# Optimization experiments

Hardware: AMD Instinct MI355X
Metric: run time of the kernel (lower is better)

Reference implementation:

```python
import jax, jax.numpy as jnp
import numpy as np

# static config (matches init_kwargs)
H = 64; W = 64; WS = 8; SHIFT = 4; HEADS = 16; DIM = 512; TED = 512; B = 16
NW = (H // WS) * (W // WS)          # 64 windows
WS2 = WS * WS                        # 64 tokens per window
N = WS2 + 1                          # +1 time-embedding token appended per window
HIDDEN = int(DIM * 4.0)


def _rel_pos_index():
    # standard Swin relative-position index over the WS*WS window tokens
    coords = np.stack(np.meshgrid(np.arange(WS), np.arange(WS), indexing='ij'))  # (2, WS, WS)
    cf = coords.reshape(2, -1)
    rel = (cf[:, :, None] - cf[:, None, :]).transpose(1, 2, 0)  # (WS2, WS2, 2)
    rel[..., 0] += WS - 1
    rel[..., 1] += WS - 1
    rel[..., 0] *= 2 * WS - 1
    return rel.sum(-1)  # (WS2, WS2) int


def _attn_mask():
    # shifted-window attention mask, exactly as built in __init__
    img_mask = np.zeros((H, W), dtype=np.float32)
    slices = (slice(0, -WS), slice(-WS, -SHIFT), slice(-SHIFT, None))
    cnt = 0
    for hs in slices:
        for ws_ in slices:
            img_mask[hs, ws_] = cnt
            cnt += 1
    mw = img_mask.reshape(H // WS, WS, W // WS, WS).transpose(0, 2, 1, 3).reshape(-1, WS2)  # (NW, WS2)
    diff = mw[:, None, :] - mw[:, :, None]
    return np.where(diff != 0, -100.0, 0.0).astype(np.float32)  # (NW, WS2, WS2)


def _ln(x, g, b):
    m = x.mean(-1, keepdims=True)
    v = ((x - m) ** 2).mean(-1, keepdims=True)
    return (x - m) / jnp.sqrt(v + 1e-5) * g + b


def setup_inputs() -> dict:
    key = jax.random.key(0)
    ks = jax.random.split(key, 10)
    s = 0.02
    return {
        'x': jax.random.normal(ks[0], (B, H * W, DIM), dtype=jnp.float32),
        'emb': jax.random.normal(ks[1], (B, TED), dtype=jnp.float32),
        'gamma1': jnp.ones((DIM,), jnp.float32),
        'beta1': jnp.zeros((DIM,), jnp.float32),
        'W_emb': jax.random.normal(ks[2], (TED, DIM), jnp.float32) * s,
        'b_emb': jnp.zeros((DIM,), jnp.float32),
        'W_qkv': jax.random.normal(ks[3], (DIM, 3 * DIM), jnp.float32) * s,
        'b_qkv': jnp.zeros((3 * DIM,), jnp.float32),
        'rel_bias_table': jax.random.normal(ks[4], ((2 * WS - 1) ** 2, HEADS), jnp.float32) * s,
        'W_proj': jax.random.normal(ks[5], (DIM, DIM), jnp.float32) * s,
        'b_proj': jnp.zeros((DIM,), jnp.float32),
        'gamma2': jnp.ones((DIM,), jnp.float32),
        'beta2': jnp.zeros((DIM,), jnp.float32),
        'W1': jax.random.normal(ks[6], (DIM, HIDDEN), jnp.float32) * s,
        'b1': jnp.zeros((HIDDEN,), jnp.float32),
        'W2': jax.random.normal(ks[7], (HIDDEN, DIM), jnp.float32) * s,
        'b2': jnp.zeros((DIM,), jnp.float32),
    }


def reference(x, emb, gamma1, beta1, W_emb, b_emb, W_qkv, b_qkv, rel_bias_table,
              W_proj, b_proj, gamma2, beta2, W1, b1, W2, b2):
    Bb, L, C = x.shape
    hd = C // HEADS
    shortcut = x
    # norm1 -> spatial -> cyclic shift
    xn = _ln(x, gamma1, beta1).reshape(Bb, H, W, C)
    xs = jnp.roll(xn, (-SHIFT, -SHIFT), axis=(1, 2))
    # window partition: (B, NW, WS2, C)
    xw = xs.reshape(Bb, H // WS, WS, W // WS, WS, C).transpose(0, 1, 3, 2, 4, 5)
    xw = xw.reshape(Bb, NW, WS2, C)
    # append time-embedding token to each window
    t = jax.nn.silu(emb) @ W_emb + b_emb                       # (B, C)
    t = jnp.broadcast_to(t[:, None, None, :], (Bb, NW, 1, C))
    xw = jnp.concatenate([xw, t], axis=2).reshape(Bb * NW, N, C)
    # windowed multi-head attention
    qkv = (xw @ W_qkv + b_qkv).reshape(Bb * NW, N, 3, HEADS, hd).transpose(2, 0, 3, 1, 4)
    q, k, v = qkv[0] * (hd ** -0.5), qkv[1], qkv[2]            # (B*NW, HEADS, N, hd)
    attn = jnp.einsum('bhnd,bhmd->bhnm', q, k)
    bias = rel_bias_table[_rel_pos_index().reshape(-1)].reshape(WS2, WS2, HEADS).transpose(2, 0, 1)
    bias = jnp.pad(bias, ((0, 0), (0, 1), (0, 1)))             # zero bias for time token
    attn = attn + bias[None]
    mask = jnp.pad(jnp.asarray(_attn_mask()), ((0, 0), (0, 1), (0, 1)))  # (NW, N, N)
    attn = attn.reshape(Bb, NW, HEADS, N, N) + mask[None, :, None]
    attn = jax.nn.softmax(attn.reshape(Bb * NW, HEADS, N, N), axis=-1)
    out = jnp.einsum('bhnm,bhmd->bnhd', attn, v).reshape(Bb * NW, N, C)
    out = (out @ W_proj + b_proj)[:, :WS2]                     # drop time token
    # window reverse + reverse shift
    out = out.reshape(Bb, H // WS, W // WS, WS, WS, C).transpose(0, 1, 3, 2, 4, 5).reshape(Bb, H, W, C)
    out = jnp.roll(out, (SHIFT, SHIFT), axis=(1, 2)).reshape(Bb, L, C)
    x1 = shortcut + out
    # norm2 + MLP (exact GELU, as torch nn.GELU default)
    hmid = jax.nn.gelu(_ln(x1, gamma2, beta2) @ W1 + b1, approximate=False)
    return x1 + hmid @ W2 + b2
```

## Files before the change

### kernel.cpp

```cpp
#include <hip/hip_runtime.h>
#include <hip/hip_bf16.h>

typedef __hip_bfloat16 bf16;
typedef short short4_t __attribute__((ext_vector_type(4)));
typedef short short8 __attribute__((ext_vector_type(8)));
typedef float f32x4 __attribute__((ext_vector_type(4)));

#define DIMC 512
#define HEADS_ 16
#define NTOK 65
#define NWIN 64
#define NB 16
#define HID 2048
#define TOTROWS 66560
#define IMGROWS 65536
#define ATT_CHUNK_WB 128
#define ATT_CHUNK_ROWS (ATT_CHUNK_WB * NTOK)


__device__ __forceinline__ float b2f(short s) {
  unsigned int u = ((unsigned int)(unsigned short)s) << 16;
  float f; __builtin_memcpy(&f, &u, 4); return f;
}
__device__ __forceinline__ short f2s(float f) {
  bf16 b = __float2bfloat16(f);
  short s; __builtin_memcpy(&s, &b, 2); return s;
}

__device__ __forceinline__ void async_lds16(const bf16* g, bf16* l) {
  __builtin_amdgcn_global_load_lds(
      (const __attribute__((address_space(1))) unsigned int*)g,
      (__attribute__((address_space(3))) unsigned int*)l,
      16, 0, 0);
}

__device__ __forceinline__ void wave_stats512(const float* v, float& m, float& rstd)
{
  float s = 0.0f, ss = 0.0f;
  #pragma unroll
  for (int e = 0; e < 8; ++e) { s += v[e]; ss += v[e] * v[e]; }
  #pragma unroll
  for (int o = 1; o < 64; o <<= 1) { s += __shfl_xor(s, o); ss += __shfl_xor(ss, o); }
  m = s * (1.0f / 512.0f);
  rstd = rsqrtf(ss * (1.0f / 512.0f) - m * m + 1e-5f);
}

__device__ __forceinline__ float gelu_t(float v) {
  float v2 = v * v;
  float a  = fmaf(0.044715f, v2, 1.0f);
  float e  = __builtin_exp2f(-2.3022042f * (v * a));
  return v * __builtin_amdgcn_rcpf(1.0f + e);
}


__global__ __launch_bounds__(256) void time_emb_kernel(
    const float* __restrict__ emb, const float* __restrict__ W_emb,
    const float* __restrict__ b_emb, float* __restrict__ t)
{
  int b = blockIdx.x;
  int c = blockIdx.y * 256 + threadIdx.x;
  __shared__ float se[512];
  for (int k = threadIdx.x; k < 512; k += 256) {
    float e = emb[b * 512 + k];
    se[k] = e / (1.0f + expf(-e));
  }
  __syncthreads();
  float acc = b_emb[c];
  for (int k = 0; k < 512; ++k) acc += se[k] * W_emb[k * 512 + c];
  t[b * 512 + c] = acc;
}

__global__ void transpose_cast_kernel(const float* __restrict__ W, bf16* __restrict__ Wt,
                                      int Kd, int Nd)
{
  __shared__ float tile[32][33];
  int n0 = blockIdx.x * 32, k0 = blockIdx.y * 32;
  for (int r = threadIdx.y; r < 32; r += 8)
    tile[r][threadIdx.x] = W[(long)(k0 + r) * Nd + n0 + threadIdx.x];
  __syncthreads();
  for (int r = threadIdx.y; r < 32; r += 8)
    Wt[(long)(n0 + r) * Kd + k0 + threadIdx.x] = __float2bfloat16(tile[threadIdx.x][r]);
}

__global__ __launch_bounds__(256) void bias_mask_kernel(
    const float* __restrict__ btab, float* __restrict__ tbl)
{
  int h = blockIdx.x, wt = blockIdx.y;
  for (int idx = threadIdx.x; idx < 6400; idx += 256) {
    int i = idx / 80, t = idx % 80;
    float v;
    if (t >= 65) v = -1e30f;
    else if (i >= 64 || t == 64) v = 0.0f;
    else {
      int rel = (((i >> 3) - (t >> 3) + 7) * 15) + ((i & 7) - (t & 7) + 7);
      v = btab[rel * HEADS_ + h];
      int rci = (wt & 2) ? (((i >> 3) < 4) ? 1 : 2) : 0;
      int cci = (wt & 1) ? (((i & 7) < 4) ? 1 : 2) : 0;
      int rct = (wt & 2) ? (((t >> 3) < 4) ? 1 : 2) : 0;
      int cct = (wt & 1) ? (((t & 7) < 4) ? 1 : 2) : 0;
      if (rci * 3 + cci != rct * 3 + cct) v -= 100.0f;
    }
    tbl[(h * 4 + wt) * 6400 + idx] = v;
  }
}

__global__ __launch_bounds__(256) void ln1_window_kernel(
    const float* __restrict__ x, const float* __restrict__ gamma,
    const float* __restrict__ beta, const float* __restrict__ t,
    bf16* __restrict__ xw)
{
  long r = (long)blockIdx.x * 4 + (threadIdx.x >> 6);
  int lane = threadIdx.x & 63;
  int wb = (int)(r / NTOK), i = (int)(r % NTOK);
  int b = wb >> 6, w = wb & 63;
  bf16* out = xw + r * 512 + lane * 8;
  if (i == 64) {
    const float* tr = t + b * 512 + lane * 8;
    short8 o;
    #pragma unroll
    for (int e = 0; e < 8; ++e) o[e] = f2s(tr[e]);
    *(short8*)out = o;
    return;
  }
  int wh = w >> 3, ww = w & 7, ih = i >> 3, iw = i & 7;
  int hsrc = ((wh * 8 + ih) + 4) & 63;
  int wsrc = ((ww * 8 + iw) + 4) & 63;
  const float* xr = x + ((long)b * 4096 + hsrc * 64 + wsrc) * 512 + lane * 8;
  float v[8];
  *(f32x4*)&v[0] = *(const f32x4*)xr;
  *(f32x4*)&v[4] = *(const f32x4*)(xr + 4);
  float m, rstd;
  wave_stats512(v, m, rstd);
  const float* g = gamma + lane * 8;
  const float* bt = beta + lane * 8;
  short8 o;
  #pragma unroll
  for (int e = 0; e < 8; ++e) o[e] = f2s((v[e] - m) * rstd * g[e] + bt[e]);
  *(short8*)out = o;
}

__global__ __launch_bounds__(256) void ln2_kernel(
    const bf16* __restrict__ x1, const float* __restrict__ gamma,
    const float* __restrict__ beta, bf16* __restrict__ out)
{
  long r = (long)blockIdx.x * 4 + (threadIdx.x >> 6);
  int lane = threadIdx.x & 63;
  short8 xv = *(const short8*)(x1 + r * 512 + lane * 8);
  float v[8];
  #pragma unroll
  for (int e = 0; e < 8; ++e) v[e] = b2f(xv[e]);
  float m, rstd;
  wave_stats512(v, m, rstd);
  const float* g = gamma + lane * 8;
  const float* bt = beta + lane * 8;
  short8 o;
  #pragma unroll
  for (int e = 0; e < 8; ++e) o[e] = f2s((v[e] - m) * rstd * g[e] + bt[e]);
  *(short8*)(out + r * 512 + lane * 8) = o;
}

template<int EPI, int K>
__global__ __launch_bounds__(512, 1) void gemm8p_kernel(
    const bf16* __restrict__ A, const bf16* __restrict__ Bt,
    const float* __restrict__ bias, int N, int nx,
    bf16* __restrict__ outB, float* __restrict__ outF,
    const float* __restrict__ xinF, const bf16* __restrict__ xinB, int rowOffset)
{
  constexpr int NKT = K / 64;
  __shared__ bf16 lds[8][128 * 64];
  const int tid = threadIdx.x;
  const int lane = tid & 63, wv = tid >> 6;
  const int wm = wv >> 2, wn = wv & 3;
  const int fr = lane & 15, fg = lane >> 4;

  const int nwg = gridDim.x, bid = blockIdx.x;
  const int q8 = nwg >> 3, rr8 = nwg & 7;
  const int xcd = bid & 7, idx = bid >> 3;
  const int sid = (xcd < rr8 ? xcd * (q8 + 1) : rr8 * (q8 + 1) + (xcd - rr8) * q8) + idx;
  const long row0 = (long)(sid / nx) * 256;
  const long col0 = (long)(sid % nx) * 256;

  const int rl = lane >> 3, sl = lane & 7;
  const int sls = sl ^ rl;

  auto stageH = [&](int buf, int mat, int h, int kt) {
    const bf16* base = mat ? Bt : A;
    const long rb = (mat ? col0 : row0) + h * 128 + wv * 8 + rl;
    const bf16* src = base + rb * (long)K + kt + sls * 8;
    bf16* dst = &lds[buf * 4 + mat * 2 + h][(wv * 8) * 64];
    async_lds16(src, dst);
    async_lds16(src + 64 * (long)K, dst + 64 * 64);
  };
  auto fragA = [&](int buf, int h, int mi, int ks) -> short8 {
    int r = wm * 64 + mi * 16 + fr;
    return *(const short8*)((const char*)&lds[buf * 4 + h][0] + r * 128 + (((ks * 4 + fg) ^ (r & 7)) << 4));
  };
  auto fragB = [&](int buf, int h, int ni, int ks) -> short8 {
    int r = wn * 32 + ni * 16 + fr;
    return *(const short8*)((const char*)&lds[buf * 4 + 2 + h][0] + r * 128 + (((ks * 4 + fg) ^ (r & 7)) << 4));
  };

  f32x4 acc[8][4] = {};
  short8 af[4][2], bvh[2][2][2];

  stageH(0, 0, 0, 0); stageH(0, 1, 0, 0); stageH(0, 1, 1, 0); stageH(0, 0, 1, 0);

  for (int t = 0; t < NKT; ++t) {
    const int buf = t & 1, nb = buf ^ 1;
    const bool st = (t + 1 < NKT);
    const int kt2 = (t + 1) << 6;

    asm volatile("s_waitcnt vmcnt(4)" ::: "memory");
    __builtin_amdgcn_s_barrier();
    #pragma unroll
    for (int mi = 0; mi < 4; ++mi) { af[mi][0] = fragA(buf, 0, mi, 0); af[mi][1] = fragA(buf, 0, mi, 1); }
    #pragma unroll
    for (int ni = 0; ni < 2; ++ni) { bvh[0][ni][0] = fragB(buf, 0, ni, 0); bvh[0][ni][1] = fragB(buf, 0, ni, 1); }
    if (st) stageH(nb, 0, 0, kt2);
    __builtin_amdgcn_s_setprio(1);
    #pragma unroll
    for (int mi = 0; mi < 4; ++mi)
      #pragma unroll
      for (int ni = 0; ni < 2; ++ni)
        #pragma unroll
        for (int ks = 0; ks < 2; ++ks)
          acc[mi][ni] = __builtin_amdgcn_mfma_f32_16x16x32_bf16(af[mi][ks], bvh[0][ni][ks], acc[mi][ni], 0, 0, 0);
    __builtin_amdgcn_s_setprio(0);

    if (st) asm volatile("s_waitcnt vmcnt(4)" ::: "memory");
    else    asm volatile("s_waitcnt vmcnt(2)" ::: "memory");
    __builtin_amdgcn_s_barrier();
    #pragma unroll
    for (int ni = 0; ni < 2; ++ni) { bvh[1][ni][0] = fragB(buf, 1, ni, 0); bvh[1][ni][1] = fragB(buf, 1, ni, 1); }
    if (st) stageH(nb, 1, 0, kt2);
    __builtin_amdgcn_s_setprio(1);
    #pragma unroll
    for (int mi = 0; mi < 4; ++mi)
      #pragma unroll
      for (int ni = 0; ni < 2; ++ni)
        #pragma unroll
        for (int ks = 0; ks < 2; ++ks)
          acc[mi][2 + ni] = __builtin_amdgcn_mfma_f32_16x16x32_bf16(af[mi][ks], bvh[1][ni][ks], acc[mi][2 + ni], 0, 0, 0);
    __builtin_amdgcn_s_setprio(0);

    if (st) asm volatile("s_waitcnt vmcnt(4)" ::: "memory");
    else    asm volatile("s_waitcnt vmcnt(0)" ::: "memory");
    __builtin_amdgcn_s_barrier();
    #pragma unroll
    for (int mi = 0; mi < 4; ++mi) { af[mi][0] = fragA(buf, 1, mi, 0); af[mi][1] = fragA(buf, 1, mi, 1); }
    if (st) { stageH(nb, 1, 1, kt2); stageH(nb, 0, 1, kt2); }
    __builtin_amdgcn_s_setprio(1);
    #pragma unroll
    for (int mi = 0; mi < 4; ++mi)
      #pragma unroll
      for (int ni = 0; ni < 2; ++ni)
        #pragma unroll
        for (int ks = 0; ks < 2; ++ks)
          acc[4 + mi][ni] = __builtin_amdgcn_mfma_f32_16x16x32_bf16(af[mi][ks], bvh[0][ni][ks], acc[4 + mi][ni], 0, 0, 0);
    #pragma unroll
    for (int mi = 0; mi < 4; ++mi)
      #pragma unroll
      for (int ni = 0; ni < 2; ++ni)
        #pragma unroll
        for (int ks = 0; ks < 2; ++ks)
          acc[4 + mi][2 + ni] = __builtin_amdgcn_mfma_f32_16x16x32_bf16(af[mi][ks], bvh[1][ni][ks], acc[4 + mi][2 + ni], 0, 0, 0);
    __builtin_amdgcn_s_setprio(0);
  }

  if (EPI == 0 || EPI == 1) {
    float bs[2][2];
    #pragma unroll
    for (int nh = 0; nh < 2; ++nh)
      #pragma unroll
      for (int ni = 0; ni < 2; ++ni)
        bs[nh][ni] = bias[col0 + nh * 128 + wn * 32 + ni * 16 + fr];
    #pragma unroll
    for (int h = 0; h < 2; ++h)
      #pragma unroll
      for (int mi = 0; mi < 4; ++mi)
        #pragma unroll
        for (int j = 0; j < 4; ++j) {
          long rr = row0 + h * 128 + wm * 64 + mi * 16 + fg * 4 + j;
          #pragma unroll
          for (int nh = 0; nh < 2; ++nh)
            #pragma unroll
            for (int ni = 0; ni < 2; ++ni) {
              long cc = col0 + nh * 128 + wn * 32 + ni * 16 + fr;
              float v = acc[h * 4 + mi][nh * 2 + ni][j] + bs[nh][ni];
              if (EPI == 1) v = gelu_t(v);
              outB[rr * N + cc] = __float2bfloat16(v);
            }
        }
    return;
  }

  __syncthreads();
  float* ep = (float*)&lds[0][0];
  const int c64 = tid & 63, r8 = tid >> 6;
  const f32x4 b4 = *(const f32x4*)&bias[col0 + c64 * 4];
  #pragma unroll
  for (int g = 0; g < 4; ++g) {
    int h = g >> 1, wmg = g & 1;
    if (wm == wmg) {
      #pragma unroll
      for (int mi = 0; mi < 4; ++mi)
        #pragma unroll
        for (int nh = 0; nh < 2; ++nh)
          #pragma unroll
          for (int ni = 0; ni < 2; ++ni)
            #pragma unroll
            for (int j = 0; j < 4; ++j)
              ep[(mi * 16 + fg * 4 + j) * 260 + nh * 128 + wn * 32 + ni * 16 + fr] =
                  acc[h * 4 + mi][nh * 2 + ni][j];
    }
    __syncthreads();
    #pragma unroll
    for (int it = 0; it < 8; ++it) {
      int lrow = it * 8 + r8;
      long rr = row0 + h * 128 + wmg * 64 + lrow;
      f32x4 v = *(const f32x4*)&ep[lrow * 260 + c64 * 4];
      v += b4;
      if (EPI == 2) {
        int grow = rowOffset + (int)rr;
        int ii = grow % NTOK;
        if (ii != 64) {
          int wb = grow / NTOK;
          int b = wb >> 6, w = wb & 63;
          int wh = w >> 3, ww = w & 7, ih = ii >> 3, iw = ii & 7;
          int hh   = ((wh * 8 + ih) + 4) & 63;
          int wcol = ((ww * 8 + iw) + 4) & 63;
          long o = ((long)b * 4096 + hh * 64 + wcol) * 512 + col0 + c64 * 4;
          f32x4 xi = *(const f32x4*)&xinF[o];
          f32x4 x1 = xi + v;
          short4_t s4;
          #pragma unroll
          for (int e = 0; e < 4; ++e) s4[e] = f2s(x1[e]);
          *(short4_t*)&outB[o] = s4;
        }
      } else {
        long o = rr * N + col0 + c64 * 4;
        short4_t xv = *(const short4_t*)&xinB[o];
        f32x4 xf;
        #pragma unroll
        for (int e = 0; e < 4; ++e) xf[e] = b2f(xv[e]);
        *(f32x4*)&outF[o] = xf + v;
      }
    }
    __syncthreads();
  }
}

template<int EPI, int K>
__global__ __launch_bounds__(256, 3) void gemmk_kernel(
    const bf16* __restrict__ A, const bf16* __restrict__ Bt,
    const float* __restrict__ bias, int N, int nx,
    bf16* __restrict__ outB, float* __restrict__ outF,
    const float* __restrict__ xinF, const bf16* __restrict__ xinB, int rowOffset)
{
  constexpr int NKT = K / 32;
  static_assert((NKT - 1) % 3 == 0, "triplet peel needs NKT = 3m+1");
  __shared__ bf16 ldsbuf[6 * 128 * 32];
  bf16* const lAp = ldsbuf;
  bf16* const lBp = ldsbuf + 3 * 4096;
  const int tid = threadIdx.x;
  const int lane = tid & 63, wv = tid >> 6;
  const int wm = wv >> 1, wn = wv & 1;
  const int fr = lane & 15, fg = lane >> 4;

  const int nwg = gridDim.x, bid = blockIdx.x;
  const int q8 = nwg >> 3, rr8 = nwg & 7;
  const int xcd = bid & 7, idx = bid >> 3;
  const int sid = (xcd < rr8 ? xcd * (q8 + 1) : rr8 * (q8 + 1) + (xcd - rr8) * q8) + idx;
  const long row0 = (long)(sid / nx) * 128;
  const long col0 = (long)(sid % nx) * 128;

  const int rl = lane >> 2, sp = lane & 3;
  const int s = sp ^ ((rl >> 1) & 3);
  const bf16* ga0 = A  + (row0 + wv * 32 + rl) * (long)K + s * 8;
  const bf16* ga1 = ga0 + 16 * (long)K;
  const bf16* gb0 = Bt + (col0 + wv * 32 + rl) * (long)K + s * 8;
  const bf16* gb1 = gb0 + 16 * (long)K;

  f32x4 acc[4][4] = {};
  const int swr = (fg ^ ((fr >> 1) & 3)) << 4;

  auto stage = [&](int buf, int t) {
    const long o = (long)t * 32;
    async_lds16(ga0 + o, &lAp[buf * 4096 + (wv * 32) * 32]);
    async_lds16(ga1 + o, &lAp[buf * 4096 + (wv * 32 + 16) * 32]);
    async_lds16(gb0 + o, &lBp[buf * 4096 + (wv * 32) * 32]);
    async_lds16(gb1 + o, &lBp[buf * 4096 + (wv * 32 + 16) * 32]);
  };

  stage(0, 0);
  stage(1, 1);

#define GBODY(BUF)                                                              \
  do {                                                                          \
    if (t + 1 < NKT) asm volatile("s_waitcnt vmcnt(4)" ::: "memory");           \
    else             asm volatile("s_waitcnt vmcnt(0)" ::: "memory");           \
    __builtin_amdgcn_s_barrier();                                               \
    short8 bfv[4], af[4];                                                       \
    _Pragma("unroll")                                                           \
    for (int ni = 0; ni < 4; ++ni)                                              \
      bfv[ni] = *(const short8*)((const char*)&lBp[(BUF) * 4096] +              \
                                 (wn * 64 + ni * 16 + fr) * 64 + swr);          \
    _Pragma("unroll")                                                           \
    for (int mi = 0; mi < 4; ++mi)                                              \
      af[mi] = *(const short8*)((const char*)&lAp[(BUF) * 4096] +               \
                                (wm * 64 + mi * 16 + fr) * 64 + swr);           \
    if (t + 2 < NKT) stage(((BUF) + 2) % 3, t + 2);                             \
    __builtin_amdgcn_s_setprio(1);                                              \
    _Pragma("unroll")                                                           \
    for (int mi = 0; mi < 4; ++mi)                                              \
      _Pragma("unroll")                                                         \
      for (int ni = 0; ni < 4; ++ni)                                            \
        acc[mi][ni] = __builtin_amdgcn_mfma_f32_16x16x32_bf16(                  \
            af[mi], bfv[ni], acc[mi][ni], 0, 0, 0);                             \
    __builtin_amdgcn_s_setprio(0);                                              \
    ++t;                                                                        \
  } while (0)

  int t = 0;
  GBODY(0);
  for (int g = 0; g < (NKT - 1) / 3; ++g) {
    GBODY(1);
    GBODY(2);
    GBODY(0);
  }
#undef GBODY

  if (EPI == 2 || EPI == 3) {
    __syncthreads();
    float* ep = (float*)ldsbuf;
    const int l31 = lane & 31, lr2 = lane >> 5;
    const f32x4 b4 = *(const f32x4*)&bias[col0 + l31 * 4];
    #pragma unroll
    for (int h = 0; h < 2; ++h) {
      if (wm == h) {
        #pragma unroll
        for (int mi = 0; mi < 4; ++mi)
          #pragma unroll
          for (int ni = 0; ni < 4; ++ni)
            #pragma unroll
            for (int j = 0; j < 4; ++j)
              ep[(mi * 16 + fg * 4 + j) * 132 + wn * 64 + ni * 16 + fr] = acc[mi][ni][j];
      }
      __syncthreads();
      #pragma unroll
      for (int it = 0; it < 8; ++it) {
        int lrow = it * 8 + wv * 2 + lr2;
        long rr = row0 + h * 64 + lrow;
        f32x4 v = *(const f32x4*)&ep[lrow * 132 + l31 * 4];
        v += b4;
        if (EPI == 2) {
          int grow = rowOffset + (int)rr;
          int ii = grow % NTOK;
          if (ii != 64) {
            int wb = grow / NTOK;
            int b = wb >> 6, w = wb & 63;
            int wh = w >> 3, ww = w & 7, ih = ii >> 3, iw = ii & 7;
            int hh   = ((wh * 8 + ih) + 4) & 63;
            int wcol = ((ww * 8 + iw) + 4) & 63;
            long o = ((long)b * 4096 + hh * 64 + wcol) * 512 + col0 + l31 * 4;
            f32x4 xi = *(const f32x4*)&xinF[o];
            f32x4 x1 = xi + v;
            short4_t s4;
            #pragma unroll
            for (int e = 0; e < 4; ++e) s4[e] = f2s(x1[e]);
            *(short4_t*)&outB[o] = s4;
          }
        } else {
          long o = rr * N + col0 + l31 * 4;
          short4_t xv = *(const short4_t*)&xinB[o];
          f32x4 xf;
          #pragma unroll
          for (int e = 0; e < 4; ++e) xf[e] = b2f(xv[e]);
          *(f32x4*)&outF[o] = xf + v;
        }
      }
      __syncthreads();
    }
    return;
  }

  float bs[4];
  #pragma unroll
  for (int ni = 0; ni < 4; ++ni) bs[ni] = bias[col0 + wn * 64 + ni * 16 + fr];
  #pragma unroll
  for (int mi = 0; mi < 4; ++mi) {
    #pragma unroll
    for (int j = 0; j < 4; ++j) {
      long rr = row0 + wm * 64 + mi * 16 + fg * 4 + j;
      #pragma unroll
      for (int ni = 0; ni < 4; ++ni) {
        long cc = col0 + wn * 64 + ni * 16 + fr;
        float v = acc[mi][ni][j] + bs[ni];
        if (EPI == 0) {
          outB[rr * N + cc] = __float2bfloat16(v);
        } else {
          outB[rr * N + cc] = __float2bfloat16(gelu_t(v));
        }
      }
    }
  }
}

__global__ __launch_bounds__(64, 4) void attn_mfma_kernel(
    const bf16* __restrict__ qkv, bf16* __restrict__ attnO,
    const float* __restrict__ tbl, int wb0)
{
  __shared__ bf16 P[80 * 104];
  const int lwb = blockIdx.x, h = blockIdx.y;
  const int lane = threadIdx.x;
  const int fr = lane & 15, g = lane >> 4;
  const float scale = 0.17677669529663687f;
  const bf16* base = qkv + (long)lwb * 65 * 1536 + h * 32 + g * 8;

  for (int idx = lane; idx < 240; idx += 64) {
    int i = idx / 3, sl = idx % 3;
    *(short8*)&P[i * 104 + 80 + sl * 8] = (short8){0, 0, 0, 0, 0, 0, 0, 0};
  }

  short8 bq[5];
  #pragma unroll
  for (int tn = 0; tn < 5; ++tn) {
    int qr = tn * 16 + fr; qr = qr > 64 ? 64 : qr;
    bq[tn] = *(const short8*)(base + (long)qr * 1536);
  }

  f32x4 acc[5][5];
  #pragma unroll
  for (int tm = 0; tm < 5; ++tm) {
    int kr = tm * 16 + fr; kr = kr > 64 ? 64 : kr;
    short8 ak = *(const short8*)(base + 512 + (long)kr * 1536);
    #pragma unroll
    for (int tn = 0; tn < 5; ++tn)
      acc[tm][tn] = __builtin_amdgcn_mfma_f32_16x16x32_bf16(
          ak, bq[tn], (f32x4){0.0f, 0.0f, 0.0f, 0.0f}, 0, 0, 0);
  }

  const int w = (wb0 + lwb) & 63;
  const int wt = (((w >> 3) == 7) ? 2 : 0) + (((w & 7) == 7) ? 1 : 0);
  const float* tp = tbl + (h * 4 + wt) * 6400;
  #pragma unroll
  for (int tn = 0; tn < 5; ++tn) {
    const int i = tn * 16 + fr;
    const float* ti = tp + i * 80 + g * 4;
    float m = -3.0e38f;
    #pragma unroll
    for (int tm = 0; tm < 5; ++tm) {
      f32x4 bvv = *(const f32x4*)(ti + tm * 16);
      #pragma unroll
      for (int r = 0; r < 4; ++r) {
        float sv = fmaf(acc[tm][tn][r], scale, bvv[r]);
        acc[tm][tn][r] = sv;
        m = fmaxf(m, sv);
      }
    }
    m = fmaxf(m, __shfl_xor(m, 16));
    m = fmaxf(m, __shfl_xor(m, 32));
    float l = 0.0f;
    #pragma unroll
    for (int tm = 0; tm < 5; ++tm)
      #pragma unroll
      for (int r = 0; r < 4; ++r) {
        float e = __expf(acc[tm][tn][r] - m);
        acc[tm][tn][r] = e;
        l += e;
      }
    l += __shfl_xor(l, 16);
    l += __shfl_xor(l, 32);
    float inv = 1.0f / l;
    #pragma unroll
    for (int tm = 0; tm < 5; ++tm) {
      short4_t pk;
      #pragma unroll
      for (int r = 0; r < 4; ++r) pk[r] = f2s(acc[tm][tn][r] * inv);
      *(short4_t*)&P[i * 104 + tm * 16 + g * 4] = pk;
    }
  }

  const bf16* vbase = qkv + (long)lwb * 65 * 1536 + 1024 + h * 32;
  f32x4 oacc[2][5] = {};
  #pragma unroll
  for (int kt = 0; kt < 3; ++kt) {
    short8 bp[5];
    #pragma unroll
    for (int tn = 0; tn < 5; ++tn)
      bp[tn] = *(const short8*)&P[(tn * 16 + fr) * 104 + kt * 32 + g * 8];
    #pragma unroll
    for (int ma = 0; ma < 2; ++ma) {
      short8 av;
      #pragma unroll
      for (int e = 0; e < 8; ++e) {
        int vr = kt * 32 + g * 8 + e; vr = vr > 64 ? 64 : vr;
        av[e] = *(const short*)(vbase + (long)vr * 1536 + ma * 16 + fr);
      }
      #pragma unroll
      for (int tn = 0; tn < 5; ++tn)
        oacc[ma][tn] = __builtin_amdgcn_mfma_f32_16x16x32_bf16(
            av, bp[tn], oacc[ma][tn], 0, 0, 0);
    }
  }

  #pragma unroll
  for (int tn = 0; tn < 5; ++tn) {
    int i = tn * 16 + fr;
    if (i < 65) {
      bf16* op = attnO + (long)(lwb * 65 + i) * 512 + h * 32 + g * 4;
      #pragma unroll
      for (int ma = 0; ma < 2; ++ma) {
        short4_t o4;
        #pragma unroll
        for (int r = 0; r < 4; ++r) o4[r] = f2s(oacc[ma][tn][r]);
        *(short4_t*)(op + ma * 16) = o4;
      }
    }
  }
}


extern "C" void kernel_launch(void* const* d_in, const int* in_sizes, int n_in,
                              void* d_out, int out_size, void* d_ws, size_t ws_size,
                              hipStream_t stream)
{
  const float* x      = (const float*)d_in[0];
  const float* emb    = (const float*)d_in[1];
  const float* gamma1 = (const float*)d_in[2];
  const float* beta1  = (const float*)d_in[3];
  const float* W_emb  = (const float*)d_in[4];
  const float* b_emb  = (const float*)d_in[5];
  const float* W_qkv  = (const float*)d_in[6];
  const float* b_qkv  = (const float*)d_in[7];
  const float* btab   = (const float*)d_in[8];
  const float* W_proj = (const float*)d_in[9];
  const float* b_proj = (const float*)d_in[10];
  const float* gamma2 = (const float*)d_in[11];
  const float* beta2  = (const float*)d_in[12];
  const float* W1     = (const float*)d_in[13];
  const float* b1     = (const float*)d_in[14];
  const float* W2     = (const float*)d_in[15];
  const float* b2     = (const float*)d_in[16];
  float* out = (float*)d_out;
  (void)n_in; (void)in_sizes; (void)out_size;

  char* ws = (char*)d_ws;
  size_t off = 0;
  auto alloc = [&](size_t bytes) -> char* {
    char* p = ws + off;
    off += (bytes + 255) & ~(size_t)255;
    return p;
  };
  bf16* wt_qkv  = (bf16*)alloc((size_t)1536 * 512 * 2);
  bf16* wt_proj = (bf16*)alloc((size_t)512 * 512 * 2);
  bf16* wt1     = (bf16*)alloc((size_t)2048 * 512 * 2);
  bf16* wt2     = (bf16*)alloc((size_t)512 * 2048 * 2);
  float* tvec   = (float*)alloc((size_t)16 * 512 * 4);
  float* tbl    = (float*)alloc((size_t)16 * 4 * 6400 * 4);

  const size_t sz_xw    = (size_t)TOTROWS * 512 * 2;
  const size_t sz_qkv   = (size_t)TOTROWS * 1536 * 2;
  const size_t sz_attnO = (size_t)TOTROWS * 512 * 2;
  const bool big = ws_size >= off + sz_xw + sz_qkv + sz_attnO + (4u << 20);

  transpose_cast_kernel<<<dim3(1536 / 32, 512 / 32), dim3(32, 8), 0, stream>>>(W_qkv, wt_qkv, 512, 1536);
  transpose_cast_kernel<<<dim3(512 / 32, 512 / 32),  dim3(32, 8), 0, stream>>>(W_proj, wt_proj, 512, 512);
  transpose_cast_kernel<<<dim3(2048 / 32, 512 / 32), dim3(32, 8), 0, stream>>>(W1, wt1, 512, 2048);
  transpose_cast_kernel<<<dim3(512 / 32, 2048 / 32), dim3(32, 8), 0, stream>>>(W2, wt2, 2048, 512);
  time_emb_kernel<<<dim3(16, 2), 256, 0, stream>>>(emb, W_emb, b_emb, tvec);
  bias_mask_kernel<<<dim3(16, 4), 256, 0, stream>>>(btab, tbl);

  if (big) {
    char* regionA = alloc(sz_xw);
    char* regionQ = alloc(sz_qkv);
    bf16* attnO   = (bf16*)alloc(sz_attnO);
    bf16* xw   = (bf16*)regionA;
    bf16* x1b  = (bf16*)regionA;
    bf16* qkv  = (bf16*)regionQ;
    bf16* h_c  = (bf16*)regionQ;
    bf16* ln2b = (bf16*)(regionQ + (size_t)32768 * 2048 * 2);

    ln1_window_kernel<<<TOTROWS / 4, 256, 0, stream>>>(x, gamma1, beta1, tvec, xw);
    gemm8p_kernel<0, 512><<<6 * 260, 512, 0, stream>>>(
        xw, wt_qkv, b_qkv, 1536, 6, qkv, nullptr, nullptr, nullptr, 0);
    attn_mfma_kernel<<<dim3(NB * NWIN, HEADS_), 64, 0, stream>>>(qkv, attnO, tbl, 0);
    gemm8p_kernel<2, 512><<<2 * 260, 512, 0, stream>>>(
        attnO, wt_proj, b_proj, 512, 2, x1b, nullptr, x, nullptr, 0);
    ln2_kernel<<<IMGROWS / 4, 256, 0, stream>>>(x1b, gamma2, beta2, ln2b);
    for (int mc = 0; mc < 2; ++mc) {
      long r0 = (long)mc * 32768;
      gemm8p_kernel<1, 512><<<8 * 128, 512, 0, stream>>>(
          ln2b + r0 * 512, wt1, b1, 2048, 8, h_c, nullptr, nullptr, nullptr, 0);
      gemm8p_kernel<3, 2048><<<2 * 128, 512, 0, stream>>>(
          h_c, wt2, b2, 512, 2, nullptr, out + r0 * 512, nullptr, x1b + r0 * 512, 0);
    }
  } else {
    char* regionA = alloc(sz_xw);
    bf16* xw   = (bf16*)regionA;
    bf16* x1b  = (bf16*)regionA;
    bf16* qkv_c = (bf16*)alloc((size_t)ATT_CHUNK_ROWS * 1536 * 2);
    char* regionB = alloc(sz_attnO);
    bf16* attnO = (bf16*)regionB;
    bf16* ln2b  = (bf16*)regionB;
    bf16* h_c   = (bf16*)alloc((size_t)16384 * 2048 * 2);

    ln1_window_kernel<<<TOTROWS / 4, 256, 0, stream>>>(x, gamma1, beta1, tvec, xw);
    for (int ac = 0; ac < 8; ++ac) {
      long r0 = (long)ac * ATT_CHUNK_ROWS;
      gemmk_kernel<0, 512><<<12 * 65, 256, 0, stream>>>(
          xw + r0 * 512, wt_qkv, b_qkv, 1536, 12, qkv_c, nullptr, nullptr, nullptr, 0);
      attn_mfma_kernel<<<dim3(ATT_CHUNK_WB, HEADS_), 64, 0, stream>>>(
          qkv_c, attnO + r0 * 512, tbl, ac * ATT_CHUNK_WB);
    }
    gemmk_kernel<2, 512><<<4 * 520, 256, 0, stream>>>(
        attnO, wt_proj, b_proj, 512, 4, x1b, nullptr, x, nullptr, 0);
    ln2_kernel<<<IMGROWS / 4, 256, 0, stream>>>(x1b, gamma2, beta2, ln2b);
    for (int mc = 0; mc < 4; ++mc) {
      long r0 = (long)mc * 16384;
      gemmk_kernel<1, 512><<<16 * 128, 256, 0, stream>>>(
          ln2b + r0 * 512, wt1, b1, 2048, 16, h_c, nullptr, nullptr, nullptr, 0);
      gemmk_kernel<3, 2048><<<4 * 128, 256, 0, stream>>>(
          h_c, wt2, b2, 512, 4, nullptr, out + r0 * 512, nullptr, x1b + r0 * 512, 0);
    }
  }
}
```

Baseline: 768.6 us.

## Switch GEMM to 4-stage K=32 pipeline with 3 tiles in flight

The main bf16 GEMM kernel now uses a K-step of 32 and a 4-buffer LDS ring, prefetching three K-tiles ahead instead of double-buffering K=64 tiles. The LDS swizzle, fragment loads and vmcnt wait counts are reworked to match, and each iteration runs two MFMA phases instead of three. The goal is to hide global-load latency with deeper prefetch and fewer barriers per unit of work. The cost is more loop iterations and barriers overall, plus fragile hand-counted waitcnt values.

```diff
diff --git a/kernel.cpp b/kernel.cpp
--- a/kernel.cpp
+++ b/kernel.cpp
@@ -166,8 +166,8 @@
     bf16* __restrict__ outB, float* __restrict__ outF,
     const float* __restrict__ xinF, const bf16* __restrict__ xinB, int rowOffset)
 {
-  constexpr int NKT = K / 64;
-  __shared__ bf16 lds[8][128 * 64];
+  constexpr int NKT = K / 32;
+  __shared__ bf16 lds[16][128 * 32];
   const int tid = threadIdx.x;
   const int lane = tid & 63, wv = tid >> 6;
   const int wm = wv >> 2, wn = wv & 3;
@@ -180,90 +180,74 @@
   const long row0 = (long)(sid / nx) * 256;
   const long col0 = (long)(sid % nx) * 256;
 
-  const int rl = lane >> 3, sl = lane & 7;
-  const int sls = sl ^ rl;
-
-  auto stageH = [&](int buf, int mat, int h, int kt) {
+  const int rl = lane >> 2, sp = lane & 3;
+  const int s = sp ^ ((rl >> 1) & 3);
+  const int swr = (fg ^ ((fr >> 1) & 3)) << 4;
+
+  auto stageHalf = [&](int buf, int mat, int h, int kt) {
     const bf16* base = mat ? Bt : A;
-    const long rb = (mat ? col0 : row0) + h * 128 + wv * 8 + rl;
-    const bf16* src = base + rb * (long)K + kt + sls * 8;
-    bf16* dst = &lds[buf * 4 + mat * 2 + h][(wv * 8) * 64];
-    async_lds16(src, dst);
-    async_lds16(src + 64 * (long)K, dst + 64 * 64);
+    const long rb = (mat ? col0 : row0) + h * 128 + wv * 16 + rl;
+    async_lds16(base + rb * (long)K + kt + s * 8,
+                &lds[buf * 4 + mat * 2 + h][(wv * 16) * 32]);
   };
-  auto fragA = [&](int buf, int h, int mi, int ks) -> short8 {
+  auto fragA = [&](int buf, int h, int mi) -> short8 {
     int r = wm * 64 + mi * 16 + fr;
-    return *(const short8*)((const char*)&lds[buf * 4 + h][0] + r * 128 + (((ks * 4 + fg) ^ (r & 7)) << 4));
+    return *(const short8*)((const char*)&lds[buf * 4 + h][0] + r * 64 + swr);
   };
-  auto fragB = [&](int buf, int h, int ni, int ks) -> short8 {
+  auto fragB = [&](int buf, int nh, int ni) -> short8 {
     int r = wn * 32 + ni * 16 + fr;
-    return *(const short8*)((const char*)&lds[buf * 4 + 2 + h][0] + r * 128 + (((ks * 4 + fg) ^ (r & 7)) << 4));
+    return *(const short8*)((const char*)&lds[buf * 4 + 2 + nh][0] + r * 64 + swr);
   };
 
   f32x4 acc[8][4] = {};
-  short8 af[4][2], bvh[2][2][2];
-
-  stageH(0, 0, 0, 0); stageH(0, 1, 0, 0); stageH(0, 1, 1, 0); stageH(0, 0, 1, 0);
+  short8 af[4], bv[4];
+
+  #pragma unroll
+  for (int p = 0; p < 3; ++p) {
+    stageHalf(p, 0, 0, p * 32);
+    stageHalf(p, 1, 0, p * 32);
+    stageHalf(p, 1, 1, p * 32);
+    stageHalf(p, 0, 1, p * 32);
+  }
 
   for (int t = 0; t < NKT; ++t) {
-    const int buf = t & 1, nb = buf ^ 1;
-    const bool st = (t + 1 < NKT);
-    const int kt2 = (t + 1) << 6;
-
-    asm volatile("s_waitcnt vmcnt(4)" ::: "memory");
+    const int buf = t & 3, nb = (t + 3) & 3;
+    const bool st = (t + 3 < NKT);
+    const int ktn = (t + 3) * 32;
+
+    if (t < NKT - 2)       asm volatile("s_waitcnt vmcnt(9)" ::: "memory");
+    else if (t == NKT - 2) asm volatile("s_waitcnt vmcnt(5)" ::: "memory");
+    else                   asm volatile("s_waitcnt vmcnt(1)" ::: "memory");
     __builtin_amdgcn_s_barrier();
     #pragma unroll
-    for (int mi = 0; mi < 4; ++mi) { af[mi][0] = fragA(buf, 0, mi, 0); af[mi][1] = fragA(buf, 0, mi, 1); }
-    #pragma unroll
-    for (int ni = 0; ni < 2; ++ni) { bvh[0][ni][0] = fragB(buf, 0, ni, 0); bvh[0][ni][1] = fragB(buf, 0, ni, 1); }
-    if (st) stageH(nb, 0, 0, kt2);
+    for (int mi = 0; mi < 4; ++mi) af[mi] = fragA(buf, 0, mi);
+    #pragma unroll
+    for (int nh = 0; nh < 2; ++nh)
+      #pragma unroll
+      for (int ni = 0; ni < 2; ++ni) bv[nh * 2 + ni] = fragB(buf, nh, ni);
+    if (st) { stageHalf(nb, 0, 0, ktn); stageHalf(nb, 1, 0, ktn); }
     __builtin_amdgcn_s_setprio(1);
     #pragma unroll
     for (int mi = 0; mi < 4; ++mi)
       #pragma unroll
-      for (int ni = 0; ni < 2; ++ni)
-        #pragma unroll
-        for (int ks = 0; ks < 2; ++ks)
-          acc[mi][ni] = __builtin_amdgcn_mfma_f32_16x16x32_bf16(af[mi][ks], bvh[0][ni][ks], acc[mi][ni], 0, 0, 0);
+      for (int np = 0; np < 4; ++np)
+        acc[mi][np] = __builtin_amdgcn_mfma_f32_16x16x32_bf16(af[mi], bv[np], acc[mi][np], 0, 0, 0);
     __builtin_amdgcn_s_setprio(0);
 
-    if (st) asm volatile("s_waitcnt vmcnt(4)" ::: "memory");
-    else    asm volatile("s_waitcnt vmcnt(2)" ::: "memory");
+    if (t < NKT - 3)       asm volatile("s_waitcnt vmcnt(10)" ::: "memory");
+    else if (t == NKT - 3) asm volatile("s_waitcnt vmcnt(8)" ::: "memory");
+    else if (t == NKT - 2) asm volatile("s_waitcnt vmcnt(4)" ::: "memory");
+    else                   asm volatile("s_waitcnt vmcnt(0)" ::: "memory");
     __builtin_amdgcn_s_barrier();
     #pragma unroll
-    for (int ni = 0; ni < 2; ++ni) { bvh[1][ni][0] = fragB(buf, 1, ni, 0); bvh[1][ni][1] = fragB(buf, 1, ni, 1); }
-    if (st) stageH(nb, 1, 0, kt2);
+    for (int mi = 0; mi < 4; ++mi) af[mi] = fragA(buf, 1, mi);
+    if (st) { stageHalf(nb, 1, 1, ktn); stageHalf(nb, 0, 1, ktn); }
     __builtin_amdgcn_s_setprio(1);
     #pragma unroll
     for (int mi = 0; mi < 4; ++mi)
       #pragma unroll
-      for (int ni = 0; ni < 2; ++ni)
-        #pragma unroll
-        for (int ks = 0; ks < 2; ++ks)
-          acc[mi][2 + ni] = __builtin_amdgcn_mfma_f32_16x16x32_bf16(af[mi][ks], bvh[1][ni][ks], acc[mi][2 + ni], 0, 0, 0);
-    __builtin_amdgcn_s_setprio(0);
-
-    if (st) asm volatile("s_waitcnt vmcnt(4)" ::: "memory");
-    else    asm volatile("s_waitcnt vmcnt(0)" ::: "memory");
-    __builtin_amdgcn_s_barrier();
-    #pragma unroll
-    for (int mi = 0; mi < 4; ++mi) { af[mi][0] = fragA(buf, 1, mi, 0); af[mi][1] = fragA(buf, 1, mi, 1); }
-    if (st) { stageH(nb, 1, 1, kt2); stageH(nb, 0, 1, kt2); }
-    __builtin_amdgcn_s_setprio(1);
-    #pragma unroll
-    for (int mi = 0; mi < 4; ++mi)
-      #pragma unroll
-      for (int ni = 0; ni < 2; ++ni)
-        #pragma unroll
-        for (int ks = 0; ks < 2; ++ks)
-          acc[4 + mi][ni] = __builtin_amdgcn_mfma_f32_16x16x32_bf16(af[mi][ks], bvh[0][ni][ks], acc[4 + mi][ni], 0, 0, 0);
-    #pragma unroll
-    for (int mi = 0; mi < 4; ++mi)
-      #pragma unroll
-      for (int ni = 0; ni < 2; ++ni)
-        #pragma unroll
-        for (int ks = 0; ks < 2; ++ks)
-          acc[4 + mi][2 + ni] = __builtin_amdgcn_mfma_f32_16x16x32_bf16(af[mi][ks], bvh[1][ni][ks], acc[4 + mi][2 + ni], 0, 0, 0);
+      for (int np = 0; np < 4; ++np)
+        acc[4 + mi][np] = __builtin_amdgcn_mfma_f32_16x16x32_bf16(af[mi], bv[np], acc[4 + mi][np], 0, 0, 0);
     __builtin_amdgcn_s_setprio(0);
   }
 
```

New measurement: 840.4 us. 9.3% more time.
